# Optimization experiments

Hardware: AMD Instinct MI355X
Metric: run time of the kernel (lower is better)

Reference implementation:

```python
import jax, jax.numpy as jnp
import numpy as np

EMBED_DIM = 1024
NUM_HEADS = 16
HEAD_DIM = EMBED_DIM // NUM_HEADS
BSZ, TGT, SRC = 4, 1024, 2048


def setup_inputs() -> dict:
    key = jax.random.key(0)
    ks = jax.random.split(key, 12)
    init = 1.0 / np.sqrt(EMBED_DIM)
    return {
        "hidden_states": jax.random.normal(ks[0], (BSZ, TGT, EMBED_DIM), jnp.float32),
        "key_value_states": jax.random.normal(ks[1], (BSZ, SRC, EMBED_DIM), jnp.float32),
        "bias": jax.random.normal(ks[2], (BSZ, NUM_HEADS, TGT, SRC), jnp.float32),
        "Wq": jax.random.normal(ks[3], (EMBED_DIM, EMBED_DIM), jnp.float32) * init,
        "bq": jax.random.normal(ks[4], (EMBED_DIM,), jnp.float32) * init,
        "Wk": jax.random.normal(ks[5], (EMBED_DIM, EMBED_DIM), jnp.float32) * init,
        "bk": jax.random.normal(ks[6], (EMBED_DIM,), jnp.float32) * init,
        "Wv": jax.random.normal(ks[7], (EMBED_DIM, EMBED_DIM), jnp.float32) * init,
        "bv": jax.random.normal(ks[8], (EMBED_DIM,), jnp.float32) * init,
        "Wo": jax.random.normal(ks[9], (EMBED_DIM, EMBED_DIM), jnp.float32) * init,
        "bo": jax.random.normal(ks[10], (EMBED_DIM,), jnp.float32) * init,
    }


def reference(hidden_states, key_value_states, bias, Wq, bq, Wk, bk, Wv, bv, Wo, bo):
    B, T, E = hidden_states.shape
    S = key_value_states.shape[1]
    H, hd = NUM_HEADS, HEAD_DIM
    scaling = hd ** (-0.5)
    # torch Linear: y = x @ W^T + b
    q = (hidden_states @ Wq.T + bq) * scaling            # [B,T,E]
    k = key_value_states @ Wk.T + bk                     # [B,S,E]
    v = key_value_states @ Wv.T + bv                     # [B,S,E]
    q = q.reshape(B, T, H, hd).transpose(0, 2, 1, 3)     # [B,H,T,hd]
    k = k.reshape(B, S, H, hd).transpose(0, 2, 1, 3)     # [B,H,S,hd]
    v = v.reshape(B, S, H, hd).transpose(0, 2, 1, 3)     # [B,H,S,hd]
    scores = jnp.einsum('bhtd,bhsd->bhts', q, k) + bias  # [B,H,T,S]
    probs = jax.nn.softmax(scores, axis=-1)
    attn = jnp.einsum('bhts,bhsd->bhtd', probs, v)       # [B,H,T,hd]
    # Faithful to the original: reshape (B*H, T, hd) -> (B, T, E) WITHOUT
    # transposing heads back (this is how the torch source does it).
    attn = attn.reshape(B, T, E)
    return attn @ Wo.T + bo
```

## Files before the change

kernel.cpp:

```cpp
#include <hip/hip_runtime.h>

#define DEVI __device__ __forceinline__

typedef __attribute__((ext_vector_type(4))) float f32x4;
typedef __attribute__((ext_vector_type(8))) short bf16x8;

DEVI unsigned short f2bf(float f) {
  unsigned int u = __builtin_bit_cast(unsigned int, f);
  u += 0x7FFFu + ((u >> 16) & 1u);
  return (unsigned short)(u >> 16);
}

DEVI void load_lds16(const void* g, void* l) {
  __builtin_amdgcn_global_load_lds(
      (__attribute__((address_space(1))) void*)g,
      (__attribute__((address_space(3))) void*)l,
      16, 0, 0);
}

struct CvtArgs {
  const float* src[6];
  unsigned short* dst[6];
  int cum[6];
};

__global__ __launch_bounds__(256) void cvt_all(CvtArgs a, int total4) {
  int i = blockIdx.x * 256 + threadIdx.x;
  if (i >= total4) return;
  int s = 0;
#pragma unroll
  for (int k = 1; k < 6; ++k) s += (i >= a.cum[k]);
  const int j = i - a.cum[s];
  const float4 v = reinterpret_cast<const float4*>(a.src[s])[j];
  ushort4 o;
  o.x = f2bf(v.x); o.y = f2bf(v.y); o.z = f2bf(v.z); o.w = f2bf(v.w);
  reinterpret_cast<ushort4*>(a.dst[s])[j] = o;
}

template<bool OUT_BF16>
DEVI void gemm_core(const unsigned short* __restrict__ A,
                    const unsigned short* __restrict__ W,
                    const float* __restrict__ bias,
                    void* __restrict__ out,
                    float scale, int log2R,
                    long sb, long st, long sh, long sd,
                    int bx, int by, bool vt)
{
  constexpr int K = 1024;
  __shared__ unsigned short smem[2 * 128 * 64];
  unsigned short* As = smem;
  unsigned short* Bs = smem + 8192;

  const int tid  = threadIdx.x;
  const int wid  = tid >> 6;
  const int lane = tid & 63;
  const int m0 = bx * 128;
  const int n0 = by * 128;
  const int wr = (wid >> 1) * 64;
  const int wc = (wid & 1) * 64;
  const int lg = lane >> 4;
  const int ll = lane & 15;

  f32x4 acc[4][4] = {};

  const char* Ab = (const char*)A + (long)m0 * K * 2;
  const char* Wb = (const char*)W + (long)n0 * K * 2;
  char* AsB = (char*)As;
  char* BsB = (char*)Bs;
  const long rowstride = (long)K * 2;

  for (int kt = 0; kt < K; kt += 64) {
#pragma unroll
    for (int j = 0; j < 4; ++j) {
      const int o    = (wid * 4 + j) * 1024 + lane * 16;
      const int row  = o >> 7;
      const int colb = o & 127;
      load_lds16(Ab + (long)row * rowstride + (long)kt * 2 + colb, AsB + (wid * 4 + j) * 1024);
      load_lds16(Wb + (long)row * rowstride + (long)kt * 2 + colb, BsB + (wid * 4 + j) * 1024);
    }
    __syncthreads();
#pragma unroll
    for (int ks = 0; ks < 2; ++ks) {
      bf16x8 af[4], bfr[4];
#pragma unroll
      for (int i = 0; i < 4; ++i) {
        af[i]  = *(const bf16x8*)&As[(wr + i * 16 + ll) * 64 + ks * 32 + lg * 8];
        bfr[i] = *(const bf16x8*)&Bs[(wc + i * 16 + ll) * 64 + ks * 32 + lg * 8];
      }
#pragma unroll
      for (int i = 0; i < 4; ++i)
#pragma unroll
        for (int j = 0; j < 4; ++j)
          acc[i][j] = __builtin_amdgcn_mfma_f32_16x16x32_bf16(af[i], bfr[j], acc[i][j], 0, 0, 0);
    }
    __syncthreads();
  }

  if (OUT_BF16 && vt) {
    const int m_base = m0 + wr;
    const int b  = m_base >> log2R;
    const int tb = m_base & ((1 << log2R) - 1);
    unsigned short* Tw = smem + wid * 2176;
#pragma unroll
    for (int h2 = 0; h2 < 2; ++h2) {
#pragma unroll
      for (int jj = 0; jj < 2; ++jj) {
        const int j = h2 * 2 + jj;
        const float bj = bias[n0 + wc + j * 16 + ll];
#pragma unroll
        for (int i = 0; i < 4; ++i)
#pragma unroll
          for (int r = 0; r < 4; ++r)
            Tw[(jj * 16 + ll) * 68 + i * 16 + lg * 4 + r] = f2bf((acc[i][j][r] + bj) * scale);
      }
      asm volatile("s_waitcnt lgkmcnt(0)" ::: "memory");
#pragma unroll
      for (int k = 0; k < 8; ++k) {
        const int dloc = k * 4 + (lane >> 4);
        const int t4   = (lane & 15) * 4;
        const ushort4 vv = *(const ushort4*)&Tw[dloc * 68 + t4];
        const int n = n0 + wc + h2 * 32 + dloc;
        const int h = n >> 6, dd = n & 63;
        *(ushort4*)((unsigned short*)out + (long)b * sb + (long)h * sh + (long)dd * sd + tb + t4) = vv;
      }
      if (h2 == 0) asm volatile("s_waitcnt lgkmcnt(0)" ::: "memory");
    }
    return;
  }

  const int Rmask = (1 << log2R) - 1;
#pragma unroll
  for (int j = 0; j < 4; ++j) {
    const int n = n0 + wc + j * 16 + ll;
    const float bj = bias[n];
    const int h = n >> 6, d = n & 63;
#pragma unroll
    for (int i = 0; i < 4; ++i) {
      const int mb = m0 + wr + i * 16 + lg * 4;
#pragma unroll
      for (int r = 0; r < 4; ++r) {
        const int m = mb + r;
        const int b = m >> log2R;
        const int t = m & Rmask;
        const long off = (long)b * sb + (long)t * st + (long)h * sh + (long)d * sd;
        const float v = (acc[i][j][r] + bj) * scale;
        if (OUT_BF16) ((unsigned short*)out)[off] = f2bf(v);
        else          ((float*)out)[off] = v;
      }
    }
  }
}

struct GemmDesc {
  const unsigned short* A;
  const unsigned short* W;
  const float* bias;
  unsigned short* out;
  float scale;
  int log2R;
  long sb, st, sh, sd;
};

__global__ __launch_bounds__(256) void gemm_qkv(GemmDesc d0, GemmDesc d1, GemmDesc d2) {
  int bid = blockIdx.x;
  const GemmDesc* d;
  bool vt = false;
  if (bid < 256)      { d = &d0; }
  else if (bid < 768) { d = &d1; bid -= 256; }
  else                { d = &d2; bid -= 768; vt = true; }
  gemm_core<true>(d->A, d->W, d->bias, d->out, d->scale, d->log2R,
                  d->sb, d->st, d->sh, d->sd, bid >> 3, bid & 7, vt);
}

__global__ __launch_bounds__(256) void gemm_o(
    const unsigned short* __restrict__ A,
    const unsigned short* __restrict__ W,
    const float* __restrict__ bias,
    float* __restrict__ out,
    long sb, long st, long sh, long sd)
{
  gemm_core<false>(A, W, bias, out, 1.0f, 10, sb, st, sh, sd, blockIdx.x, blockIdx.y, false);
}

__global__ __launch_bounds__(256) void attn_fused(
    const unsigned short* __restrict__ Qb,
    const unsigned short* __restrict__ Kb,
    const unsigned short* __restrict__ Vt,
    const float* __restrict__ bias,
    unsigned short* __restrict__ Ob)
{
  constexpr int T = 1024, S = 2048;
  __shared__ unsigned short Ks[64 * 72];
  __shared__ unsigned short Vs[64 * 72];
  __shared__ unsigned short Ps[4][32 * 72];

  const int tid = threadIdx.x;
  const int w = tid >> 6, lane = tid & 63;
  const int lg = lane >> 4, ll = lane & 15;
  const int t0 = blockIdx.x * 128;
  const int bh = blockIdx.z * 16 + blockIdx.y;

  bf16x8 qf[2][2];
#pragma unroll
  for (int rf = 0; rf < 2; ++rf)
#pragma unroll
    for (int ks = 0; ks < 2; ++ks)
      qf[rf][ks] = *(const bf16x8*)(Qb + ((long)bh * T + t0 + w * 32 + rf * 16 + ll) * 64 + ks * 32 + lg * 8);

  f32x4 acc[2][4] = {};
  f32x4 m_run[2], l_run[2];
#pragma unroll
  for (int rf = 0; rf < 2; ++rf)
#pragma unroll
    for (int r = 0; r < 4; ++r) { m_run[rf][r] = -1e30f; l_run[rf][r] = 0.0f; }

  const char* Kg = (const char*)(Kb + (long)bh * S * 64);
  const char* Vg = (const char*)(Vt + (long)bh * 64 * S);
  const float* biasg = bias + ((long)bh * T + t0) * S;

  for (int sc = 0; sc < S / 64; ++sc) {
#pragma unroll
    for (int r2 = 0; r2 < 2; ++r2) {
      const int o = (tid + r2 * 256) * 16;
      const int row = o >> 7, colb = o & 127;
      uint4 kd = *(const uint4*)(Kg + (long)(sc * 64 + row) * 128 + colb);
      *(uint4*)((char*)&Ks[0] + row * 144 + colb) = kd;
      uint4 vd = *(const uint4*)(Vg + (long)row * (S * 2) + sc * 128 + colb);
      *(uint4*)((char*)&Vs[0] + row * 144 + colb) = vd;
    }
    __syncthreads();

    f32x4 sv[2][4] = {};
#pragma unroll
    for (int ks = 0; ks < 2; ++ks) {
      bf16x8 kf[4];
#pragma unroll
      for (int sf = 0; sf < 4; ++sf)
        kf[sf] = *(const bf16x8*)((const char*)&Ks[0] + (sf * 16 + ll) * 144 + (ks * 32 + lg * 8) * 2);
#pragma unroll
      for (int rf = 0; rf < 2; ++rf)
#pragma unroll
        for (int sf = 0; sf < 4; ++sf)
          sv[rf][sf] = __builtin_amdgcn_mfma_f32_16x16x32_bf16(qf[rf][ks], kf[sf], sv[rf][sf], 0, 0, 0);
    }

#pragma unroll
    for (int rf = 0; rf < 2; ++rf) {
      const int trow = w * 32 + rf * 16 + lg * 4;
#pragma unroll
      for (int sf = 0; sf < 4; ++sf) {
        const long bo_ = (long)trow * S + sc * 64 + sf * 16 + ll;
#pragma unroll
        for (int r = 0; r < 4; ++r)
          sv[rf][sf][r] += biasg[bo_ + (long)r * S];
      }
      f32x4 rmax;
#pragma unroll
      for (int r = 0; r < 4; ++r)
        rmax[r] = fmaxf(fmaxf(sv[rf][0][r], sv[rf][1][r]), fmaxf(sv[rf][2][r], sv[rf][3][r]));
#pragma unroll
      for (int off = 1; off < 16; off <<= 1)
#pragma unroll
        for (int r = 0; r < 4; ++r)
          rmax[r] = fmaxf(rmax[r], __shfl_xor(rmax[r], off));
      f32x4 mnew, alpha, rsum;
#pragma unroll
      for (int r = 0; r < 4; ++r) {
        mnew[r]  = fmaxf(m_run[rf][r], rmax[r]);
        alpha[r] = __expf(m_run[rf][r] - mnew[r]);
        rsum[r]  = 0.0f;
      }
#pragma unroll
      for (int sf = 0; sf < 4; ++sf)
#pragma unroll
        for (int r = 0; r < 4; ++r) {
          const float p = __expf(sv[rf][sf][r] - mnew[r]);
          sv[rf][sf][r] = p;
          rsum[r] += p;
        }
#pragma unroll
      for (int off = 1; off < 16; off <<= 1)
#pragma unroll
        for (int r = 0; r < 4; ++r)
          rsum[r] += __shfl_xor(rsum[r], off);
#pragma unroll
      for (int r = 0; r < 4; ++r) {
        l_run[rf][r] = l_run[rf][r] * alpha[r] + rsum[r];
        m_run[rf][r] = mnew[r];
      }
#pragma unroll
      for (int df = 0; df < 4; ++df)
#pragma unroll
        for (int r = 0; r < 4; ++r)
          acc[rf][df][r] *= alpha[r];
      unsigned short* Pw = &Ps[w][0];
#pragma unroll
      for (int sf = 0; sf < 4; ++sf)
#pragma unroll
        for (int r = 0; r < 4; ++r)
          Pw[(rf * 16 + lg * 4 + r) * 72 + sf * 16 + ll] = f2bf(sv[rf][sf][r]);
    }

    asm volatile("s_waitcnt lgkmcnt(0)" ::: "memory");

#pragma unroll
    for (int ks = 0; ks < 2; ++ks) {
      bf16x8 pa[2], vf[4];
#pragma unroll
      for (int rf = 0; rf < 2; ++rf)
        pa[rf] = *(const bf16x8*)((const char*)&Ps[w][0] + (rf * 16 + ll) * 144 + (ks * 32 + lg * 8) * 2);
#pragma unroll
      for (int df = 0; df < 4; ++df)
        vf[df] = *(const bf16x8*)((const char*)&Vs[0] + (df * 16 + ll) * 144 + (ks * 32 + lg * 8) * 2);
#pragma unroll
      for (int rf = 0; rf < 2; ++rf)
#pragma unroll
        for (int df = 0; df < 4; ++df)
          acc[rf][df] = __builtin_amdgcn_mfma_f32_16x16x32_bf16(pa[rf], vf[df], acc[rf][df], 0, 0, 0);
    }
    __syncthreads();
  }

#pragma unroll
  for (int rf = 0; rf < 2; ++rf) {
    f32x4 inv;
#pragma unroll
    for (int r = 0; r < 4; ++r) inv[r] = 1.0f / l_run[rf][r];
#pragma unroll
    for (int df = 0; df < 4; ++df)
#pragma unroll
      for (int r = 0; r < 4; ++r) {
        const long oo = ((long)bh * T + t0 + w * 32 + rf * 16 + lg * 4 + r) * 64 + df * 16 + ll;
        Ob[oo] = f2bf(acc[rf][df][r] * inv[r]);
      }
  }
}

extern "C" void kernel_launch(void* const* d_in, const int* in_sizes, int n_in,
                              void* d_out, int out_size, void* d_ws, size_t ws_size,
                              hipStream_t stream) {
  constexpr int B = 4, T = 1024, S = 2048, E = 1024;
  const float* hs   = (const float*)d_in[0];
  const float* kv   = (const float*)d_in[1];
  const float* bias = (const float*)d_in[2];
  const float* Wq   = (const float*)d_in[3];
  const float* bq   = (const float*)d_in[4];
  const float* Wk   = (const float*)d_in[5];
  const float* bk   = (const float*)d_in[6];
  const float* Wv   = (const float*)d_in[7];
  const float* bv   = (const float*)d_in[8];
  const float* Wo   = (const float*)d_in[9];
  const float* bo   = (const float*)d_in[10];

  char* ws = (char*)d_ws;
  const size_t MB = 1024 * 1024;
  unsigned short* hs_bf = (unsigned short*)(ws);
  unsigned short* kv_bf = (unsigned short*)(ws + 8 * MB);
  unsigned short* wq_bf = (unsigned short*)(ws + 24 * MB);
  unsigned short* wk_bf = (unsigned short*)(ws + 26 * MB);
  unsigned short* wv_bf = (unsigned short*)(ws + 28 * MB);
  unsigned short* wo_bf = (unsigned short*)(ws + 30 * MB);
  unsigned short* q_buf = (unsigned short*)(ws + 32 * MB);
  unsigned short* k_buf = (unsigned short*)(ws + 40 * MB);
  unsigned short* v_buf = (unsigned short*)(ws + 56 * MB);
  unsigned short* a_buf = (unsigned short*)(ws + 72 * MB);

  CvtArgs ca;
  ca.src[0] = hs;  ca.dst[0] = hs_bf;
  ca.src[1] = kv;  ca.dst[1] = kv_bf;
  ca.src[2] = Wq;  ca.dst[2] = wq_bf;
  ca.src[3] = Wk;  ca.dst[3] = wk_bf;
  ca.src[4] = Wv;  ca.dst[4] = wv_bf;
  ca.src[5] = Wo;  ca.dst[5] = wo_bf;
  const int n4_hs = B * T * E / 4, n4_kv = B * S * E / 4, n4_w = E * E / 4;
  ca.cum[0] = 0;
  ca.cum[1] = n4_hs;
  ca.cum[2] = n4_hs + n4_kv;
  ca.cum[3] = n4_hs + n4_kv + n4_w;
  ca.cum[4] = n4_hs + n4_kv + 2 * n4_w;
  ca.cum[5] = n4_hs + n4_kv + 3 * n4_w;
  const int total4 = n4_hs + n4_kv + 4 * n4_w;
  cvt_all<<<dim3((total4 + 255) / 256), dim3(256), 0, stream>>>(ca, total4);

  GemmDesc dq{hs_bf, wq_bf, bq, q_buf, 0.125f, 10,
              (long)T * E, 64L, (long)T * 64, 1L};
  GemmDesc dk{kv_bf, wk_bf, bk, k_buf, 1.0f, 11,
              (long)S * E, 64L, (long)S * 64, 1L};
  GemmDesc dv{kv_bf, wv_bf, bv, v_buf, 1.0f, 11,
              (long)S * E, 1L, (long)S * 64, (long)S};
  gemm_qkv<<<dim3(1280), 256, 0, stream>>>(dq, dk, dv);

  attn_fused<<<dim3(T / 128, 16, B), 256, 0, stream>>>(q_buf, k_buf, v_buf, bias, a_buf);

  gemm_o<<<dim3(32, 8), 256, 0, stream>>>(
      a_buf, wo_bf, bo, (float*)d_out,
      (long)T * E, (long)E, 64L, 1L);
}
```

Before: 306.1 us.

## Transpose attention QK^T for vectorized bias loads, shrink tiles, add XCD swizzle

The attention kernel now computes S^T (K as the A operand), so each lane holds four consecutive source columns of one query row. The fp32 bias can then be read with float4 loads, and the row max and sum reduce in two cross-lane shuffles instead of four. Each block now covers 64 query rows (16 per wave) instead of 128, which doubles the grid. Launch bounds request higher occupancy. XCD-aware block remapping is added to the attention, QKV and output GEMM kernels to improve L2 locality, at the cost of more K/V reloads per query row.

Measured after the change: 306.3 us. No clear change (+0.0%).

```diff
diff --git a/kernel.cpp b/kernel.cpp
--- a/kernel.cpp
+++ b/kernel.cpp
@@ -17,6 +17,8 @@
       (__attribute__((address_space(3))) void*)l,
       16, 0, 0);
 }
+
+DEVI int xcd_swz(int bid, int chunk) { return (bid & 7) * chunk + (bid >> 3); }
 
 struct CvtArgs {
   const float* src[6];
@@ -162,7 +164,7 @@
 };
 
 __global__ __launch_bounds__(256) void gemm_qkv(GemmDesc d0, GemmDesc d1, GemmDesc d2) {
-  int bid = blockIdx.x;
+  int bid = xcd_swz(blockIdx.x, 160);
   const GemmDesc* d;
   bool vt = false;
   if (bid < 256)      { d = &d0; }
@@ -179,10 +181,11 @@
     float* __restrict__ out,
     long sb, long st, long sh, long sd)
 {
-  gemm_core<false>(A, W, bias, out, 1.0f, 10, sb, st, sh, sd, blockIdx.x, blockIdx.y, false);
-}
-
-__global__ __launch_bounds__(256) void attn_fused(
+  const int bid = xcd_swz(blockIdx.x, 32);
+  gemm_core<false>(A, W, bias, out, 1.0f, 10, sb, st, sh, sd, bid >> 3, bid & 7, false);
+}
+
+__global__ __launch_bounds__(256, 4) void attn_fused(
     const unsigned short* __restrict__ Qb,
     const unsigned short* __restrict__ Kb,
     const unsigned short* __restrict__ Vt,
@@ -192,31 +195,30 @@
   constexpr int T = 1024, S = 2048;
   __shared__ unsigned short Ks[64 * 72];
   __shared__ unsigned short Vs[64 * 72];
-  __shared__ unsigned short Ps[4][32 * 72];
+  __shared__ unsigned short Ps[4][16 * 72];
 
   const int tid = threadIdx.x;
   const int w = tid >> 6, lane = tid & 63;
   const int lg = lane >> 4, ll = lane & 15;
-  const int t0 = blockIdx.x * 128;
-  const int bh = blockIdx.z * 16 + blockIdx.y;
-
-  bf16x8 qf[2][2];
-#pragma unroll
-  for (int rf = 0; rf < 2; ++rf)
-#pragma unroll
-    for (int ks = 0; ks < 2; ++ks)
-      qf[rf][ks] = *(const bf16x8*)(Qb + ((long)bh * T + t0 + w * 32 + rf * 16 + ll) * 64 + ks * 32 + lg * 8);
-
-  f32x4 acc[2][4] = {};
-  f32x4 m_run[2], l_run[2];
-#pragma unroll
-  for (int rf = 0; rf < 2; ++rf)
-#pragma unroll
-    for (int r = 0; r < 4; ++r) { m_run[rf][r] = -1e30f; l_run[rf][r] = 0.0f; }
+
+  const int wg = xcd_swz(blockIdx.x, 128);
+  const int bh = wg >> 4;
+  const int tt = wg & 15;
+  const int t0 = tt * 64;
+  const int trow = t0 + w * 16;
+
+  bf16x8 qf[2];
+#pragma unroll
+  for (int ks = 0; ks < 2; ++ks)
+    qf[ks] = *(const bf16x8*)(Qb + ((long)bh * T + trow + ll) * 64 + ks * 32 + lg * 8);
+
+  f32x4 acc[4] = {};
+  float m_run = -1e30f, l_run = 0.0f;
 
   const char* Kg = (const char*)(Kb + (long)bh * S * 64);
   const char* Vg = (const char*)(Vt + (long)bh * 64 * S);
   const float* biasg = bias + ((long)bh * T + t0) * S;
+  const float* bias_row = biasg + (long)(w * 16 + ll) * S + lg * 4;
 
   for (int sc = 0; sc < S / 64; ++sc) {
 #pragma unroll
@@ -230,7 +232,7 @@
     }
     __syncthreads();
 
-    f32x4 sv[2][4] = {};
+    f32x4 sv[4] = {};
 #pragma unroll
     for (int ks = 0; ks < 2; ++ks) {
       bf16x8 kf[4];
@@ -238,102 +240,85 @@
       for (int sf = 0; sf < 4; ++sf)
         kf[sf] = *(const bf16x8*)((const char*)&Ks[0] + (sf * 16 + ll) * 144 + (ks * 32 + lg * 8) * 2);
 #pragma unroll
-      for (int rf = 0; rf < 2; ++rf)
-#pragma unroll
-        for (int sf = 0; sf < 4; ++sf)
-          sv[rf][sf] = __builtin_amdgcn_mfma_f32_16x16x32_bf16(qf[rf][ks], kf[sf], sv[rf][sf], 0, 0, 0);
-    }
-
-#pragma unroll
-    for (int rf = 0; rf < 2; ++rf) {
-      const int trow = w * 32 + rf * 16 + lg * 4;
-#pragma unroll
-      for (int sf = 0; sf < 4; ++sf) {
-        const long bo_ = (long)trow * S + sc * 64 + sf * 16 + ll;
-#pragma unroll
-        for (int r = 0; r < 4; ++r)
-          sv[rf][sf][r] += biasg[bo_ + (long)r * S];
-      }
-      f32x4 rmax;
-#pragma unroll
-      for (int r = 0; r < 4; ++r)
-        rmax[r] = fmaxf(fmaxf(sv[rf][0][r], sv[rf][1][r]), fmaxf(sv[rf][2][r], sv[rf][3][r]));
-#pragma unroll
-      for (int off = 1; off < 16; off <<= 1)
-#pragma unroll
-        for (int r = 0; r < 4; ++r)
-          rmax[r] = fmaxf(rmax[r], __shfl_xor(rmax[r], off));
-      f32x4 mnew, alpha, rsum;
+      for (int sf = 0; sf < 4; ++sf)
+        sv[sf] = __builtin_amdgcn_mfma_f32_16x16x32_bf16(kf[sf], qf[ks], sv[sf], 0, 0, 0);
+    }
+
+    const float* bp = bias_row + sc * 64;
+#pragma unroll
+    for (int sf = 0; sf < 4; ++sf) {
+      const float4 b4 = *(const float4*)(bp + sf * 16);
+      sv[sf][0] += b4.x; sv[sf][1] += b4.y; sv[sf][2] += b4.z; sv[sf][3] += b4.w;
+    }
+
+    float cm = sv[0][0];
+#pragma unroll
+    for (int sf = 0; sf < 4; ++sf)
+#pragma unroll
+      for (int r = 0; r < 4; ++r) cm = fmaxf(cm, sv[sf][r]);
+    cm = fmaxf(cm, __shfl_xor(cm, 16));
+    cm = fmaxf(cm, __shfl_xor(cm, 32));
+
+    const float mnew = fmaxf(m_run, cm);
+    const float alpha = __expf(m_run - mnew);
+    float ps = 0.0f;
+#pragma unroll
+    for (int sf = 0; sf < 4; ++sf)
 #pragma unroll
       for (int r = 0; r < 4; ++r) {
-        mnew[r]  = fmaxf(m_run[rf][r], rmax[r]);
-        alpha[r] = __expf(m_run[rf][r] - mnew[r]);
-        rsum[r]  = 0.0f;
-      }
-#pragma unroll
-      for (int sf = 0; sf < 4; ++sf)
-#pragma unroll
-        for (int r = 0; r < 4; ++r) {
-          const float p = __expf(sv[rf][sf][r] - mnew[r]);
-          sv[rf][sf][r] = p;
-          rsum[r] += p;
-        }
-#pragma unroll
-      for (int off = 1; off < 16; off <<= 1)
-#pragma unroll
-        for (int r = 0; r < 4; ++r)
-          rsum[r] += __shfl_xor(rsum[r], off);
-#pragma unroll
-      for (int r = 0; r < 4; ++r) {
-        l_run[rf][r] = l_run[rf][r] * alpha[r] + rsum[r];
-        m_run[rf][r] = mnew[r];
-      }
-#pragma unroll
-      for (int df = 0; df < 4; ++df)
-#pragma unroll
-        for (int r = 0; r < 4; ++r)
-          acc[rf][df][r] *= alpha[r];
-      unsigned short* Pw = &Ps[w][0];
-#pragma unroll
-      for (int sf = 0; sf < 4; ++sf)
-#pragma unroll
-        for (int r = 0; r < 4; ++r)
-          Pw[(rf * 16 + lg * 4 + r) * 72 + sf * 16 + ll] = f2bf(sv[rf][sf][r]);
-    }
-
+        const float p = __expf(sv[sf][r] - mnew);
+        sv[sf][r] = p;
+        ps += p;
+      }
+    ps += __shfl_xor(ps, 16);
+    ps += __shfl_xor(ps, 32);
+    l_run = l_run * alpha + ps;
+    m_run = mnew;
+
+    float ar[4];
+#pragma unroll
+    for (int r = 0; r < 4; ++r) ar[r] = __shfl(alpha, lg * 4 + r);
+#pragma unroll
+    for (int df = 0; df < 4; ++df)
+#pragma unroll
+      for (int r = 0; r < 4; ++r) acc[df][r] *= ar[r];
+
+    unsigned short* Pw = &Ps[w][0];
+#pragma unroll
+    for (int sf = 0; sf < 4; ++sf) {
+      ushort4 pw;
+      pw.x = f2bf(sv[sf][0]); pw.y = f2bf(sv[sf][1]);
+      pw.z = f2bf(sv[sf][2]); pw.w = f2bf(sv[sf][3]);
+      *(ushort4*)&Pw[ll * 72 + sf * 16 + lg * 4] = pw;
+    }
     asm volatile("s_waitcnt lgkmcnt(0)" ::: "memory");
+    __builtin_amdgcn_sched_barrier(0);
 
 #pragma unroll
     for (int ks = 0; ks < 2; ++ks) {
-      bf16x8 pa[2], vf[4];
-#pragma unroll
-      for (int rf = 0; rf < 2; ++rf)
-        pa[rf] = *(const bf16x8*)((const char*)&Ps[w][0] + (rf * 16 + ll) * 144 + (ks * 32 + lg * 8) * 2);
+      bf16x8 pa = *(const bf16x8*)((const char*)Pw + ll * 144 + ks * 64 + lg * 16);
+      bf16x8 vf[4];
 #pragma unroll
       for (int df = 0; df < 4; ++df)
         vf[df] = *(const bf16x8*)((const char*)&Vs[0] + (df * 16 + ll) * 144 + (ks * 32 + lg * 8) * 2);
 #pragma unroll
-      for (int rf = 0; rf < 2; ++rf)
-#pragma unroll
-        for (int df = 0; df < 4; ++df)
-          acc[rf][df] = __builtin_amdgcn_mfma_f32_16x16x32_bf16(pa[rf], vf[df], acc[rf][df], 0, 0, 0);
+      for (int df = 0; df < 4; ++df)
+        acc[df] = __builtin_amdgcn_mfma_f32_16x16x32_bf16(pa, vf[df], acc[df], 0, 0, 0);
     }
     __syncthreads();
   }
 
-#pragma unroll
-  for (int rf = 0; rf < 2; ++rf) {
-    f32x4 inv;
-#pragma unroll
-    for (int r = 0; r < 4; ++r) inv[r] = 1.0f / l_run[rf][r];
-#pragma unroll
-    for (int df = 0; df < 4; ++df)
-#pragma unroll
-      for (int r = 0; r < 4; ++r) {
-        const long oo = ((long)bh * T + t0 + w * 32 + rf * 16 + lg * 4 + r) * 64 + df * 16 + ll;
-        Ob[oo] = f2bf(acc[rf][df][r] * inv[r]);
-      }
-  }
+  const float inv = 1.0f / l_run;
+  float ir[4];
+#pragma unroll
+  for (int r = 0; r < 4; ++r) ir[r] = __shfl(inv, lg * 4 + r);
+#pragma unroll
+  for (int df = 0; df < 4; ++df)
+#pragma unroll
+    for (int r = 0; r < 4; ++r) {
+      const long oo = ((long)bh * T + trow + lg * 4 + r) * 64 + df * 16 + ll;
+      Ob[oo] = f2bf(acc[df][r] * ir[r]);
+    }
 }
 
 extern "C" void kernel_launch(void* const* d_in, const int* in_sizes, int n_in,
@@ -390,9 +375,9 @@
               (long)S * E, 1L, (long)S * 64, (long)S};
   gemm_qkv<<<dim3(1280), 256, 0, stream>>>(dq, dk, dv);
 
-  attn_fused<<<dim3(T / 128, 16, B), 256, 0, stream>>>(q_buf, k_buf, v_buf, bias, a_buf);
-
-  gemm_o<<<dim3(32, 8), 256, 0, stream>>>(
+  attn_fused<<<dim3(1024), 256, 0, stream>>>(q_buf, k_buf, v_buf, bias, a_buf);
+
+  gemm_o<<<dim3(256), 256, 0, stream>>>(
       a_buf, wo_bf, bo, (float*)d_out,
       (long)T * E, (long)E, 64L, 1L);
 }
```
